# Kernel optimization log

Measured on AMD Instinct MI355X. Metric: run time of the kernel, lower is better.

## Reference

```python
import jax, jax.numpy as jnp
import numpy as np

B, DIM, L = 16, 1024, 1024
EPS = 1e-12  # F.normalize eps


def l2norm(x, axis=1):
    # torch F.normalize: x / clamp_min(||x||_2, eps)
    n = jnp.sqrt(jnp.sum(x * x, axis=axis, keepdims=True))
    return x / jnp.maximum(n, EPS)


def setup_inputs() -> dict:
    key = jax.random.key(0)
    ks = jax.random.split(key, 8)
    inp = {
        "V": jax.random.normal(ks[0], (B, DIM, L), dtype=jnp.float32),
        "T": jax.random.normal(ks[1], (B, DIM, L), dtype=jnp.float32),
    }
    scale = 1.0 / np.sqrt(DIM)
    names = ["WQ1", "WK1", "WV1", "Wq2", "Wk2", "Wv2"]
    for i, nme in enumerate(names):
        inp[nme] = jax.random.normal(ks[2 + i], (DIM, DIM), dtype=jnp.float32) * scale
    return inp


def reference(V, T, WQ1, WK1, WV1, Wq2, Wk2, Wv2):
    # V, T: [B, dim, L]
    T = l2norm(T, axis=1)                      # normalize over feature dim
    Vt = jnp.swapaxes(V, -2, -1)               # [B, L, dim]
    Tt = jnp.swapaxes(T, -2, -1)               # [B, L, dim]

    relu = jax.nn.relu
    q1 = relu(jnp.einsum('bld,ed->ble', Vt, WQ1))
    k1 = relu(jnp.einsum('bld,ed->ble', Tt, WK1))
    v1 = relu(jnp.einsum('bld,ed->ble', Tt, WV1))
    q2 = relu(jnp.einsum('bld,ed->ble', Tt, Wq2))
    k2 = relu(jnp.einsum('bld,ed->ble', Vt, Wk2))
    v2 = relu(jnp.einsum('bld,ed->ble', Vt, Wv2))

    inv_sqrt_d = 1.0 / jnp.sqrt(jnp.asarray(DIM, dtype=q1.dtype))

    s1 = jnp.einsum('bqd,bkd->bqk', q1, k1) * inv_sqrt_d   # [B, Lv, Lt]
    p1 = jax.nn.softmax(s1, axis=1)                        # softmax over query axis (dim=1)
    w1 = jnp.einsum('bqk,bkd->bqd', p1, v1)                # [B, Lv, dim]
    cV = l2norm(V + jnp.swapaxes(w1, -2, -1), axis=1)      # [B, dim, Lv]

    s2 = jnp.einsum('bqd,bkd->bqk', q2, k2) * inv_sqrt_d   # [B, Lt, Lv]
    p2 = jax.nn.softmax(s2, axis=1)
    w2 = jnp.einsum('bqk,bkd->bqd', p2, v2)                # [B, Lt, dim]
    cT = l2norm(T + jnp.swapaxes(w2, -2, -1), axis=1)      # [B, dim, Lt]

    return l2norm(cV + cT, axis=1)
```

## Files before the change

kernel.cpp:

```cpp
#include <hip/hip_runtime.h>

#define L 1024
#define DIM 1024
#define NB 16

typedef unsigned short u16;
typedef __attribute__((ext_vector_type(4))) float f32x4;
typedef __attribute__((ext_vector_type(8))) short s16x8;

__device__ __forceinline__ float bf2f(u16 x){
  union { unsigned u; float f; } c; c.u = ((unsigned)x) << 16; return c.f;
}
__device__ __forceinline__ u16 f2bf(float f){
  union { float f; unsigned u; } c; c.f = f;
  unsigned r = c.u + 0x7fffu + ((c.u >> 16) & 1u);
  return (u16)(r >> 16);
}
__device__ __forceinline__ void gload_lds16(const void* g, void* l){
  __builtin_amdgcn_global_load_lds(
      (const __attribute__((address_space(1))) void*)g,
      (__attribute__((address_space(3))) void*)l, 16, 0, 0);
}

struct WPtrs { const float* p[6]; };

__global__ __launch_bounds__(256) void k_wconv(WPtrs wp, u16* out){
  long idx = (long)blockIdx.x * blockDim.x + threadIdx.x;
  long base = idx * 4;
  int w = (int)(base >> 20);
  long off = base & ((1 << 20) - 1);
  float4 v = *(const float4*)(wp.p[w] + off);
  ushort4 o;
  o.x = f2bf(v.x); o.y = f2bf(v.y); o.z = f2bf(v.z); o.w = f2bf(v.w);
  *(ushort4*)(out + base) = o;
}

__global__ __launch_bounds__(256) void k_transpose(const float* X, u16* Xt, int bo){
  __shared__ u16 tile[64][68];
  int b = blockIdx.y;
  int d0 = (blockIdx.x >> 4) * 64;
  int l0 = (blockIdx.x & 15) * 64;
  const float* Xb = X + (long)(bo + b) * DIM * L;
  u16* Xtb = Xt + (long)b * L * DIM;
  int q = threadIdx.x & 15, g = threadIdx.x >> 4;
  for (int r = g; r < 64; r += 16){
    float4 v = *(const float4*)(Xb + (long)(d0 + r) * L + l0 + q * 4);
    ushort4 h; h.x = f2bf(v.x); h.y = f2bf(v.y); h.z = f2bf(v.z); h.w = f2bf(v.w);
    *(ushort4*)&tile[r][q * 4] = h;
  }
  __syncthreads();
  for (int r = g; r < 64; r += 16){
    ushort4 h;
    h.x = tile[q * 4 + 0][r]; h.y = tile[q * 4 + 1][r];
    h.z = tile[q * 4 + 2][r]; h.w = tile[q * 4 + 3][r];
    *(ushort4*)&Xtb[(long)(l0 + r) * DIM + d0 + q * 4] = h;
  }
}

__global__ __launch_bounds__(256) void k_tnorm(const float* T_, u16* Tnt, float* rT,
                                               float* Z1, float* Z2, int bo){
  __shared__ float red[16][16][5];
  __shared__ float rn[64];
  __shared__ u16 tile[64][68];
  int b = blockIdx.y; int l0 = blockIdx.x * 64;
  const float* Tb = T_ + (long)(bo + b) * DIM * L;
  int q = threadIdx.x & 15, g = threadIdx.x >> 4;
  if (threadIdx.x < 64){
    Z1[(long)b * L + l0 + threadIdx.x] = 0.f;
    Z2[(long)b * L + l0 + threadIdx.x] = 0.f;
  }
  f32x4 ss = {0.f, 0.f, 0.f, 0.f};
  for (int d = g; d < DIM; d += 16){
    float4 v = *(const float4*)(Tb + (long)d * L + l0 + q * 4);
    f32x4 vv = {v.x, v.y, v.z, v.w};
    ss += vv * vv;
  }
  #pragma unroll
  for (int e = 0; e < 4; e++) red[g][q][e] = ss[e];
  __syncthreads();
  if (threadIdx.x < 64){
    int c = threadIdx.x;
    float n = 0.f;
    #pragma unroll
    for (int gg = 0; gg < 16; gg++) n += red[gg][c >> 2][c & 3];
    float r = 1.0f / fmaxf(sqrtf(n), 1e-12f);
    rn[c] = r;
    rT[(long)b * L + l0 + c] = r;
  }
  __syncthreads();
  float r0 = rn[q * 4], r1 = rn[q * 4 + 1], r2 = rn[q * 4 + 2], r3 = rn[q * 4 + 3];
  u16* Tntb = Tnt + (long)b * L * DIM;
  for (int ch = 0; ch < 16; ch++){
    int dbase = ch * 64;
    for (int r = g; r < 64; r += 16){
      float4 v = *(const float4*)(Tb + (long)(dbase + r) * L + l0 + q * 4);
      ushort4 h;
      h.x = f2bf(v.x * r0); h.y = f2bf(v.y * r1);
      h.z = f2bf(v.z * r2); h.w = f2bf(v.w * r3);
      *(ushort4*)&tile[r][q * 4] = h;
    }
    __syncthreads();
    for (int r = g; r < 64; r += 16){
      ushort4 h;
      h.x = tile[q * 4 + 0][r]; h.y = tile[q * 4 + 1][r];
      h.z = tile[q * 4 + 2][r]; h.w = tile[q * 4 + 3][r];
      *(ushort4*)&Tntb[(long)(l0 + r) * DIM + dbase + q * 4] = h;
    }
    __syncthreads();
  }
}


struct GemmDesc {
  const u16* A[4]; const u16* B[4]; u16* C[4];
  float* Z[4];
  long sA[4], sB[4], sC[4];
  int epi[4];
  float scale;
};

#define VM6 asm volatile("s_waitcnt vmcnt(6)" ::: "memory")
#define VM8 asm volatile("s_waitcnt vmcnt(8)" ::: "memory")
#define VM4 asm volatile("s_waitcnt vmcnt(4)" ::: "memory")
#define VM0 asm volatile("s_waitcnt vmcnt(0)" ::: "memory")

#define PH(slot, mq, nq, LA, LB, STAGE, WAITC) do {                           \
  if (LA){                                                                    \
    _Pragma("unroll")                                                         \
    for (int f = 0; f < 4; f++){                                              \
      av[f][0] = *(const s16x8*)&lds[(slot)*16384 + arow + (mq)*4096 + f*1024 + cko0]; \
      av[f][1] = *(const s16x8*)&lds[(slot)*16384 + arow + (mq)*4096 + f*1024 + cko1]; \
    }                                                                         \
  }                                                                           \
  if (LB){                                                                    \
    _Pragma("unroll")                                                         \
    for (int g2 = 0; g2 < 2; g2++){                                           \
      bv[nq][g2][0] = *(const s16x8*)&lds[32768 + (slot)*16384 + brow + (nq)*2048 + g2*1024 + cko0]; \
      bv[nq][g2][1] = *(const s16x8*)&lds[32768 + (slot)*16384 + brow + (nq)*2048 + g2*1024 + cko1]; \
    }                                                                         \
  }                                                                           \
  STAGE;                                                                      \
  WAITC;                                                                      \
  __builtin_amdgcn_s_barrier();                                               \
  asm volatile("s_waitcnt lgkmcnt(0)" ::: "memory");                          \
  __builtin_amdgcn_s_setprio(1);                                              \
  _Pragma("unroll")                                                           \
  for (int f = 0; f < 4; f++)                                                 \
    _Pragma("unroll")                                                         \
    for (int g2 = 0; g2 < 2; g2++){                                           \
      acc[(mq)*4+f][(nq)*2+g2] = __builtin_amdgcn_mfma_f32_16x16x32_bf16(     \
          av[f][0], bv[nq][g2][0], acc[(mq)*4+f][(nq)*2+g2], 0, 0, 0);        \
      acc[(mq)*4+f][(nq)*2+g2] = __builtin_amdgcn_mfma_f32_16x16x32_bf16(     \
          av[f][1], bv[nq][g2][1], acc[(mq)*4+f][(nq)*2+g2], 0, 0, 0);        \
    }                                                                         \
  __builtin_amdgcn_s_setprio(0);                                              \
  __builtin_amdgcn_s_barrier();                                               \
} while(0)

__global__ __launch_bounds__(512, 2) void k_gemmM(GemmDesc gd, int shift){
  constexpr int K = 1024, NN = 1024, NT = K / 64, NIT = NT / 2;
  __shared__ u16 lds[65536];

  int tid = threadIdx.x;
  int w = tid >> 6, l = tid & 63;
  int wr = w >> 2, wc = w & 3;
  int lr = l & 15, cb = l >> 4;

  int nwg = gridDim.x, cpx = nwg >> 3;
  int swz = (blockIdx.x & 7) * cpx + (blockIdx.x >> 3);
  int mat = swz >> shift;
  int local = swz & ((1 << shift) - 1);
  int batch = local >> 4;
  int tile = local & 15;
  int bm = (tile >> 2) * 256, bn = (tile & 3) * 256;

  const u16* Ab = gd.A[mat] + (long)batch * gd.sA[mat] + (long)bm * K;
  const u16* Bb = gd.B[mat] + (long)batch * gd.sB[mat] + (long)bn * K;
  int epi = gd.epi[mat];

  int arow = (wr * 128 + lr) * 64;
  int brow = (wc * 64 + lr) * 64;
  int cko0 = ((cb) ^ (lr & 7)) * 8;
  int cko1 = ((4 + cb) ^ (lr & 7)) * 8;

  int srow8 = l >> 3;
  int schunk = (l & 7) ^ (l >> 3);

  auto stA = [&](int slot, int t, int q){
    #pragma unroll
    for (int j = 0; j < 2; j++){
      int wb = w * 2 + j;
      int gr = ((wb >> 3) * 128) + ((wb & 7) * 8) + q * 64;
      gload_lds16(Ab + (long)(gr + srow8) * K + t * 64 + schunk * 8,
                  (u16*)lds + slot * 16384 + gr * 64);
    }
  };
  auto stB = [&](int slot, int t, int q){
    #pragma unroll
    for (int j = 0; j < 2; j++){
      int wb = w * 2 + j;
      int gr = ((wb >> 2) * 64) + ((wb & 3) * 8) + q * 32;
      gload_lds16(Bb + (long)(gr + srow8) * K + t * 64 + schunk * 8,
                  (u16*)lds + 32768 + slot * 16384 + gr * 64);
    }
  };

  f32x4 acc[8][4] = {};
  s16x8 av[4][2];
  s16x8 bv[2][2][2];

  stA(0, 0, 0); stB(0, 0, 0); stA(0, 0, 1); stB(0, 0, 1);
  stA(1, 1, 0); stB(1, 1, 0);
  VM8;
  __builtin_amdgcn_s_barrier();

  #pragma unroll 1
  for (int i = 0; i < NIT - 1; ++i){
    int t1 = 2 * i + 1, t2 = 2 * i + 2, t3 = 2 * i + 3;
    PH(0, 0, 0, 1, 1, stA(1, t1, 1), VM6);
    PH(0, 0, 1, 0, 1, stB(1, t1, 1), (void)0);
    PH(0, 1, 0, 1, 0, stA(0, t2, 0), (void)0);
    PH(0, 1, 1, 0, 0, stB(0, t2, 0), VM8);
    PH(1, 0, 0, 1, 1, stA(0, t2, 1), VM6);
    PH(1, 0, 1, 0, 1, stB(0, t2, 1), (void)0);
    PH(1, 1, 0, 1, 0, stA(1, t3, 0), (void)0);
    PH(1, 1, 1, 0, 0, stB(1, t3, 0), VM8);
  }
  {
    int t1 = NT - 1;
    PH(0, 0, 0, 1, 1, stA(1, t1, 1), VM6);
    PH(0, 0, 1, 0, 1, stB(1, t1, 1), (void)0);
    PH(0, 1, 0, 1, 0, (void)0, (void)0);
    PH(0, 1, 1, 0, 0, (void)0, VM4);
    PH(1, 0, 0, 1, 1, (void)0, VM0);
    PH(1, 0, 1, 0, 1, (void)0, (void)0);
    PH(1, 1, 0, 1, 0, (void)0, (void)0);
    PH(1, 1, 1, 0, 0, (void)0, (void)0);
  }

  u16* Cb = gd.C[mat] + (long)batch * gd.sC[mat];
  float sc = gd.scale;
  float iz[4];
  if (epi == 2){
    const float* Zp = gd.Z[mat] + (long)batch * NN;
    #pragma unroll
    for (int j = 0; j < 4; j++) iz[j] = 1.0f / Zp[bn + wc * 64 + j * 16 + lr];
  }
  float cs[4] = {0.f, 0.f, 0.f, 0.f};
  int cb4 = cb * 4;
  #pragma unroll
  for (int ai = 0; ai < 8; ai++)
    #pragma unroll
    for (int j = 0; j < 4; j++)
      #pragma unroll
      for (int r = 0; r < 4; r++){
        float v = acc[ai][j][r];
        if (epi == 0) v = fmaxf(v, 0.f);
        else if (epi == 1){ v = __expf(v * sc); cs[j] += v; }
        else if (epi == 2) v = fmaxf(v, 0.f) * iz[j];
        int row = bm + wr * 128 + ai * 16 + cb4 + r;
        int col = bn + wc * 64 + j * 16 + lr;
        Cb[(long)row * NN + col] = f2bf(v);
      }
  if (epi == 1){
    float* Zp = gd.Z[mat] + (long)batch * NN;
    #pragma unroll
    for (int j = 0; j < 4; j++){
      float c = cs[j];
      c += __shfl_xor(c, 16);
      c += __shfl_xor(c, 32);
      if (l < 16) atomicAdd(&Zp[bn + wc * 64 + j * 16 + l], c);
    }
  }
}

__global__ __launch_bounds__(1024) void k_final(const float* V, const float* T_,
                                                const float* rT, const u16* w1t,
                                                const u16* w2t, float* out, int bo){
  __shared__ float red[64][16][13];
  __shared__ float fac[3][64];
  int b = blockIdx.y;
  int c0 = blockIdx.x * 64;
  long gbase = (long)(bo + b) * DIM * L + c0;
  long lbase = (long)b * DIM * L + c0;
  int cq = threadIdx.x & 15, g = threadIdx.x >> 4;
  int coff = cq * 4;
  float4 rt4 = *(const float4*)(rT + (long)b * L + c0 + coff);
  f32x4 rtv = {rt4.x, rt4.y, rt4.z, rt4.w};
  f32x4 s1 = {0.f,0.f,0.f,0.f}, s2 = {0.f,0.f,0.f,0.f}, s12 = {0.f,0.f,0.f,0.f};
  #pragma unroll 4
  for (int d = g; d < DIM; d += 64){
    long o = (long)d * L + coff;
    float4 v = *(const float4*)(V + gbase + o);
    float4 t = *(const float4*)(T_ + gbase + o);
    ushort4 w1 = *(const ushort4*)(w1t + lbase + o);
    ushort4 w2 = *(const ushort4*)(w2t + lbase + o);
    f32x4 a = {v.x + bf2f(w1.x), v.y + bf2f(w1.y), v.z + bf2f(w1.z), v.w + bf2f(w1.w)};
    f32x4 tt = {t.x, t.y, t.z, t.w};
    f32x4 bb = tt * rtv;
    bb[0] += bf2f(w2.x); bb[1] += bf2f(w2.y); bb[2] += bf2f(w2.z); bb[3] += bf2f(w2.w);
    s1 += a * a; s2 += bb * bb; s12 += a * bb;
  }
  #pragma unroll
  for (int e = 0; e < 4; e++){
    red[g][cq][e] = s1[e];
    red[g][cq][4 + e] = s2[e];
    red[g][cq][8 + e] = s12[e];
  }
  __syncthreads();
  if (threadIdx.x < 192){
    int q = threadIdx.x / 12, s = threadIdx.x % 12;
    float acc = 0.f;
    #pragma unroll 8
    for (int gg = 0; gg < 64; gg++) acc += red[gg][q][s];
    red[0][q][s] = acc;
  }
  __syncthreads();
  if (threadIdx.x < 64){
    int c = threadIdx.x;
    float n1 = red[0][c >> 2][c & 3];
    float n2 = red[0][c >> 2][4 + (c & 3)];
    float cc = red[0][c >> 2][8 + (c & 3)];
    float rn1 = 1.f / fmaxf(sqrtf(n1), 1e-12f);
    float rn2 = 1.f / fmaxf(sqrtf(n2), 1e-12f);
    float n3 = n1 * rn1 * rn1 + 2.f * cc * rn1 * rn2 + n2 * rn2 * rn2;
    float rn3 = 1.f / fmaxf(sqrtf(n3), 1e-12f);
    fac[0][c] = rn1; fac[1][c] = rn2; fac[2][c] = rn3;
  }
  __syncthreads();
  f32x4 f1, f2, f3;
  #pragma unroll
  for (int e = 0; e < 4; e++){
    f1[e] = fac[0][coff + e]; f2[e] = fac[1][coff + e]; f3[e] = fac[2][coff + e];
  }
  #pragma unroll 4
  for (int d = g; d < DIM; d += 64){
    long o = (long)d * L + coff;
    float4 v = *(const float4*)(V + gbase + o);
    float4 t = *(const float4*)(T_ + gbase + o);
    ushort4 w1 = *(const ushort4*)(w1t + lbase + o);
    ushort4 w2 = *(const ushort4*)(w2t + lbase + o);
    f32x4 a = {v.x + bf2f(w1.x), v.y + bf2f(w1.y), v.z + bf2f(w1.z), v.w + bf2f(w1.w)};
    f32x4 tt = {t.x, t.y, t.z, t.w};
    f32x4 bb = tt * rtv;
    bb[0] += bf2f(w2.x); bb[1] += bf2f(w2.y); bb[2] += bf2f(w2.z); bb[3] += bf2f(w2.w);
    f32x4 r = (a * f1 + bb * f2) * f3;
    float4 st = {r[0], r[1], r[2], r[3]};
    *(float4*)(out + gbase + o) = st;
  }
}

extern "C" void kernel_launch(void* const* d_in, const int* in_sizes, int n_in,
                              void* d_out, int out_size, void* d_ws, size_t ws_size,
                              hipStream_t stream) {
  const float* V = (const float*)d_in[0];
  const float* T = (const float*)d_in[1];
  char* ws = (char*)d_ws;
  const long MB = 1 << 20;
  float* out = (float*)d_out;

  int G = NB;
  while (G > 1 && (size_t)((13 + 14 * (long)G) * MB) > ws_size) G >>= 1;
  int shift = 4 + (31 - __builtin_clz((unsigned)G));

  u16*   Wb  = (u16*)(ws);
  float* rT  = (float*)(ws + 12 * MB);
  float* Z1  = (float*)(ws + 12 * MB + 128 * 1024);
  float* Z2  = (float*)(ws + 12 * MB + 256 * 1024);
  char*  bufs = ws + 13 * MB;
  long   BUF  = (long)G * 2 * MB;
  u16* S0 = (u16*)(bufs + 0 * BUF);
  u16* S1 = (u16*)(bufs + 1 * BUF);
  u16* S2 = (u16*)(bufs + 2 * BUF);
  u16* S3 = (u16*)(bufs + 3 * BUF);
  u16* S4 = (u16*)(bufs + 4 * BUF);
  u16* S5 = (u16*)(bufs + 5 * BUF);
  u16* S6 = (u16*)(bufs + 6 * BUF);

  WPtrs wp;
  for (int i = 0; i < 6; i++) wp.p[i] = (const float*)d_in[2 + i];
  const u16* WQ1 = Wb + 0L * MB; const u16* WK1 = Wb + 1L * MB;
  const u16* WV1 = Wb + 2L * MB; const u16* Wq2 = Wb + 3L * MB;
  const u16* Wk2 = Wb + 4L * MB; const u16* Wv2 = Wb + 5L * MB;

  long LD = (long)L * DIM;
  const float invsq = 0.03125f;

  u16* Vt = S0, *Tnt = S1;
  u16* k1 = S2, *q2 = S3, *q1 = S4, *k2 = S5;
  u16* E1 = S6, *E2 = S4;
  u16* v1 = S2, *v2 = S5;
  u16* w1b = S3, *w2b = S0;

  GemmDesc g1 = {};
  g1.A[0] = Vt;  g1.B[0] = WQ1; g1.C[0] = q1;
  g1.A[1] = Tnt; g1.B[1] = WK1; g1.C[1] = k1;
  g1.A[2] = Tnt; g1.B[2] = Wq2; g1.C[2] = q2;
  g1.A[3] = Vt;  g1.B[3] = Wk2; g1.C[3] = k2;
  for (int i = 0; i < 4; i++){ g1.sA[i] = LD; g1.sB[i] = 0; g1.sC[i] = LD;
    g1.epi[i] = 0; g1.Z[i] = Z1; }
  g1.scale = 0.f;

  GemmDesc ge = {};
  ge.A[0] = q1; ge.B[0] = k1; ge.C[0] = E1; ge.Z[0] = Z1;
  ge.A[1] = q2; ge.B[1] = k2; ge.C[1] = E2; ge.Z[1] = Z2;
  ge.A[2] = q1; ge.B[2] = k1; ge.C[2] = E1; ge.Z[2] = Z1;
  ge.A[3] = q1; ge.B[3] = k1; ge.C[3] = E1; ge.Z[3] = Z1;
  for (int i = 0; i < 4; i++){ ge.sA[i] = LD; ge.sB[i] = LD; ge.sC[i] = LD; ge.epi[i] = 1; }
  ge.scale = invsq;

  GemmDesc gv = {};
  gv.A[0] = WV1; gv.B[0] = Tnt; gv.C[0] = v1; gv.Z[0] = Z1;
  gv.A[1] = Wv2; gv.B[1] = Vt;  gv.C[1] = v2; gv.Z[1] = Z2;
  gv.A[2] = WV1; gv.B[2] = Tnt; gv.C[2] = v1; gv.Z[2] = Z1;
  gv.A[3] = WV1; gv.B[3] = Tnt; gv.C[3] = v1; gv.Z[3] = Z1;
  for (int i = 0; i < 4; i++){ gv.sA[i] = 0; gv.sB[i] = LD; gv.sC[i] = LD; gv.epi[i] = 2; }
  gv.scale = 0.f;

  GemmDesc g4 = {};
  g4.A[0] = v1; g4.B[0] = E1; g4.C[0] = w1b; g4.Z[0] = Z1;
  g4.A[1] = v2; g4.B[1] = E2; g4.C[1] = w2b; g4.Z[1] = Z2;
  g4.A[2] = v1; g4.B[2] = E1; g4.C[2] = w1b; g4.Z[2] = Z1;
  g4.A[3] = v1; g4.B[3] = E1; g4.C[3] = w1b; g4.Z[3] = Z1;
  for (int i = 0; i < 4; i++){ g4.sA[i] = LD; g4.sB[i] = LD; g4.sC[i] = LD; g4.epi[i] = 3; }
  g4.scale = 0.f;

  k_wconv<<<6144, 256, 0, stream>>>(wp, Wb);

  for (int bo = 0; bo < NB; bo += G){
    k_transpose<<<dim3(256, G), 256, 0, stream>>>(V, Vt, bo);
    k_tnorm<<<dim3(16, G), 256, 0, stream>>>(T, Tnt, rT, Z1, Z2, bo);

    k_gemmM<<<4 * 16 * G, 512, 0, stream>>>(g1, shift);
    k_gemmM<<<2 * 16 * G, 512, 0, stream>>>(ge, shift);
    k_gemmM<<<2 * 16 * G, 512, 0, stream>>>(gv, shift);
    k_gemmM<<<2 * 16 * G, 512, 0, stream>>>(g4, shift);

    k_final<<<dim3(16, G), 1024, 0, stream>>>(V, T, rT, w1b, w2b, out, bo);
  }
}
```

Before: 579.7 us.

## Merge transpose and T-norm prep; split final normalization across D halves

Fuses the V transpose and T normalization kernels into one launch, using block-index ranges to pick the role. The final L2-normalization kernel is split into a reduction kernel and an apply kernel, each covering half the feature dimension via a z-grid. Partial norms are combined through global atomics into new P1/P2/P3 buffers, which the prep kernel zeroes. This doubles the block count to raise occupancy on a small grid, at the cost of an extra launch, atomics, and re-reading V/T/w1/w2 in the apply pass.

New measurement: 580.0 us. No clear change (+0.1%).

```diff
diff --git a/kernel.cpp b/kernel.cpp
--- a/kernel.cpp
+++ b/kernel.cpp
@@ -35,39 +35,42 @@
   *(ushort4*)(out + base) = o;
 }
 
-__global__ __launch_bounds__(256) void k_transpose(const float* X, u16* Xt, int bo){
+__global__ __launch_bounds__(256) void k_prep(const float* V, const float* T_,
+                                              u16* Vt, u16* Tnt, float* rT,
+                                              float* Z1, float* Z2,
+                                              float* P1, float* P2, float* P3, int bo){
   __shared__ u16 tile[64][68];
-  int b = blockIdx.y;
-  int d0 = (blockIdx.x >> 4) * 64;
-  int l0 = (blockIdx.x & 15) * 64;
-  const float* Xb = X + (long)(bo + b) * DIM * L;
-  u16* Xtb = Xt + (long)b * L * DIM;
-  int q = threadIdx.x & 15, g = threadIdx.x >> 4;
-  for (int r = g; r < 64; r += 16){
-    float4 v = *(const float4*)(Xb + (long)(d0 + r) * L + l0 + q * 4);
-    ushort4 h; h.x = f2bf(v.x); h.y = f2bf(v.y); h.z = f2bf(v.z); h.w = f2bf(v.w);
-    *(ushort4*)&tile[r][q * 4] = h;
-  }
-  __syncthreads();
-  for (int r = g; r < 64; r += 16){
-    ushort4 h;
-    h.x = tile[q * 4 + 0][r]; h.y = tile[q * 4 + 1][r];
-    h.z = tile[q * 4 + 2][r]; h.w = tile[q * 4 + 3][r];
-    *(ushort4*)&Xtb[(long)(l0 + r) * DIM + d0 + q * 4] = h;
-  }
-}
-
-__global__ __launch_bounds__(256) void k_tnorm(const float* T_, u16* Tnt, float* rT,
-                                               float* Z1, float* Z2, int bo){
   __shared__ float red[16][16][5];
   __shared__ float rn[64];
-  __shared__ u16 tile[64][68];
-  int b = blockIdx.y; int l0 = blockIdx.x * 64;
+  int b = blockIdx.y;
+  int q = threadIdx.x & 15, g = threadIdx.x >> 4;
+
+  if (blockIdx.x < 256){
+    int d0 = (blockIdx.x >> 4) * 64;
+    int l0 = (blockIdx.x & 15) * 64;
+    const float* Xb = V + (long)(bo + b) * DIM * L;
+    u16* Xtb = Vt + (long)b * L * DIM;
+    for (int r = g; r < 64; r += 16){
+      float4 v = *(const float4*)(Xb + (long)(d0 + r) * L + l0 + q * 4);
+      ushort4 h; h.x = f2bf(v.x); h.y = f2bf(v.y); h.z = f2bf(v.z); h.w = f2bf(v.w);
+      *(ushort4*)&tile[r][q * 4] = h;
+    }
+    __syncthreads();
+    for (int r = g; r < 64; r += 16){
+      ushort4 h;
+      h.x = tile[q * 4 + 0][r]; h.y = tile[q * 4 + 1][r];
+      h.z = tile[q * 4 + 2][r]; h.w = tile[q * 4 + 3][r];
+      *(ushort4*)&Xtb[(long)(l0 + r) * DIM + d0 + q * 4] = h;
+    }
+    return;
+  }
+
+  int l0 = (blockIdx.x - 256) * 64;
   const float* Tb = T_ + (long)(bo + b) * DIM * L;
-  int q = threadIdx.x & 15, g = threadIdx.x >> 4;
   if (threadIdx.x < 64){
-    Z1[(long)b * L + l0 + threadIdx.x] = 0.f;
-    Z2[(long)b * L + l0 + threadIdx.x] = 0.f;
+    long o = (long)b * L + l0 + threadIdx.x;
+    Z1[o] = 0.f; Z2[o] = 0.f;
+    P1[o] = 0.f; P2[o] = 0.f; P3[o] = 0.f;
   }
   f32x4 ss = {0.f, 0.f, 0.f, 0.f};
   for (int d = g; d < DIM; d += 16){
@@ -109,7 +112,6 @@
     __syncthreads();
   }
 }
-
 
 struct GemmDesc {
   const u16* A[4]; const u16* B[4]; u16* C[4];
@@ -274,13 +276,14 @@
   }
 }
 
-__global__ __launch_bounds__(1024) void k_final(const float* V, const float* T_,
-                                                const float* rT, const u16* w1t,
-                                                const u16* w2t, float* out, int bo){
+__global__ __launch_bounds__(1024, 8) void k_fred(const float* V, const float* T_,
+                                                  const float* rT, const u16* w1t,
+                                                  const u16* w2t,
+                                                  float* P1, float* P2, float* P3, int bo){
   __shared__ float red[64][16][13];
-  __shared__ float fac[3][64];
   int b = blockIdx.y;
   int c0 = blockIdx.x * 64;
+  int dbeg = blockIdx.z * 512;
   long gbase = (long)(bo + b) * DIM * L + c0;
   long lbase = (long)b * DIM * L + c0;
   int cq = threadIdx.x & 15, g = threadIdx.x >> 4;
@@ -288,8 +291,8 @@
   float4 rt4 = *(const float4*)(rT + (long)b * L + c0 + coff);
   f32x4 rtv = {rt4.x, rt4.y, rt4.z, rt4.w};
   f32x4 s1 = {0.f,0.f,0.f,0.f}, s2 = {0.f,0.f,0.f,0.f}, s12 = {0.f,0.f,0.f,0.f};
-  #pragma unroll 4
-  for (int d = g; d < DIM; d += 64){
+  #pragma unroll 2
+  for (int d = dbeg + g; d < dbeg + 512; d += 64){
     long o = (long)d * L + coff;
     float4 v = *(const float4*)(V + gbase + o);
     float4 t = *(const float4*)(T_ + gbase + o);
@@ -308,33 +311,65 @@
     red[g][cq][8 + e] = s12[e];
   }
   __syncthreads();
+  if (g < 32){
+    #pragma unroll
+    for (int e = 0; e < 12; e++) red[g][cq][e] += red[g + 32][cq][e];
+  }
+  __syncthreads();
+  if (g < 16){
+    #pragma unroll
+    for (int e = 0; e < 12; e++) red[g][cq][e] += red[g + 16][cq][e];
+  }
+  __syncthreads();
+  if (g < 8){
+    #pragma unroll
+    for (int e = 0; e < 12; e++) red[g][cq][e] += red[g + 8][cq][e];
+  }
+  __syncthreads();
   if (threadIdx.x < 192){
     int q = threadIdx.x / 12, s = threadIdx.x % 12;
     float acc = 0.f;
-    #pragma unroll 8
-    for (int gg = 0; gg < 64; gg++) acc += red[gg][q][s];
-    red[0][q][s] = acc;
-  }
-  __syncthreads();
+    #pragma unroll
+    for (int gg = 0; gg < 8; gg++) acc += red[gg][q][s];
+    int which = s >> 2, e = s & 3;
+    long col = (long)b * L + c0 + q * 4 + e;
+    float* P = which == 0 ? P1 : (which == 1 ? P2 : P3);
+    atomicAdd(&P[col], acc);
+  }
+}
+
+__global__ __launch_bounds__(1024, 8) void k_fapply(const float* V, const float* T_,
+                                                    const float* rT, const u16* w1t,
+                                                    const u16* w2t,
+                                                    const float* P1, const float* P2,
+                                                    const float* P3, float* out, int bo){
+  __shared__ float fac[3][64];
+  int b = blockIdx.y;
+  int c0 = blockIdx.x * 64;
+  int dbeg = blockIdx.z * 512;
+  long gbase = (long)(bo + b) * DIM * L + c0;
+  long lbase = (long)b * DIM * L + c0;
+  int cq = threadIdx.x & 15, g = threadIdx.x >> 4;
+  int coff = cq * 4;
   if (threadIdx.x < 64){
-    int c = threadIdx.x;
-    float n1 = red[0][c >> 2][c & 3];
-    float n2 = red[0][c >> 2][4 + (c & 3)];
-    float cc = red[0][c >> 2][8 + (c & 3)];
+    long col = (long)b * L + c0 + threadIdx.x;
+    float n1 = P1[col], n2 = P2[col], cc = P3[col];
     float rn1 = 1.f / fmaxf(sqrtf(n1), 1e-12f);
     float rn2 = 1.f / fmaxf(sqrtf(n2), 1e-12f);
     float n3 = n1 * rn1 * rn1 + 2.f * cc * rn1 * rn2 + n2 * rn2 * rn2;
     float rn3 = 1.f / fmaxf(sqrtf(n3), 1e-12f);
-    fac[0][c] = rn1; fac[1][c] = rn2; fac[2][c] = rn3;
-  }
-  __syncthreads();
+    fac[0][threadIdx.x] = rn1; fac[1][threadIdx.x] = rn2; fac[2][threadIdx.x] = rn3;
+  }
+  __syncthreads();
+  float4 rt4 = *(const float4*)(rT + (long)b * L + c0 + coff);
+  f32x4 rtv = {rt4.x, rt4.y, rt4.z, rt4.w};
   f32x4 f1, f2, f3;
   #pragma unroll
   for (int e = 0; e < 4; e++){
     f1[e] = fac[0][coff + e]; f2[e] = fac[1][coff + e]; f3[e] = fac[2][coff + e];
   }
-  #pragma unroll 4
-  for (int d = g; d < DIM; d += 64){
+  #pragma unroll 2
+  for (int d = dbeg + g; d < dbeg + 512; d += 64){
     long o = (long)d * L + coff;
     float4 v = *(const float4*)(V + gbase + o);
     float4 t = *(const float4*)(T_ + gbase + o);
@@ -367,6 +402,9 @@
   float* rT  = (float*)(ws + 12 * MB);
   float* Z1  = (float*)(ws + 12 * MB + 128 * 1024);
   float* Z2  = (float*)(ws + 12 * MB + 256 * 1024);
+  float* P1  = (float*)(ws + 12 * MB + 384 * 1024);
+  float* P2  = (float*)(ws + 12 * MB + 512 * 1024);
+  float* P3  = (float*)(ws + 12 * MB + 640 * 1024);
   char*  bufs = ws + 13 * MB;
   long   BUF  = (long)G * 2 * MB;
   u16* S0 = (u16*)(bufs + 0 * BUF);
@@ -428,14 +466,14 @@
   k_wconv<<<6144, 256, 0, stream>>>(wp, Wb);
 
   for (int bo = 0; bo < NB; bo += G){
-    k_transpose<<<dim3(256, G), 256, 0, stream>>>(V, Vt, bo);
-    k_tnorm<<<dim3(16, G), 256, 0, stream>>>(T, Tnt, rT, Z1, Z2, bo);
+    k_prep<<<dim3(272, G), 256, 0, stream>>>(V, T, Vt, Tnt, rT, Z1, Z2, P1, P2, P3, bo);
 
     k_gemmM<<<4 * 16 * G, 512, 0, stream>>>(g1, shift);
     k_gemmM<<<2 * 16 * G, 512, 0, stream>>>(ge, shift);
     k_gemmM<<<2 * 16 * G, 512, 0, stream>>>(gv, shift);
     k_gemmM<<<2 * 16 * G, 512, 0, stream>>>(g4, shift);
 
-    k_final<<<dim3(16, G), 1024, 0, stream>>>(V, T, rT, w1b, w2b, out, bo);
-  }
-}
+    k_fred<<<dim3(16, G, 2), 1024, 0, stream>>>(V, T, rT, w1b, w2b, P1, P2, P3, bo);
+    k_fapply<<<dim3(16, G, 2), 1024, 0, stream>>>(V, T, rT, w1b, w2b, P1, P2, P3, out, bo);
+  }
+}
```
